# Kernel optimization log

Hardware: AMD Instinct MI355X
Metric: run time of the kernel (lower is better)

The kernel has to match this reference:

```python
import jax, jax.numpy as jnp
import numpy as np

LSP_ORDER = 32
RATE = 0.01
N_ITER = 4
MIN_D = RATE * np.pi / (LSP_ORDER + 1)  # _precompute


def setup_inputs() -> dict:
    key = jax.random.key(0)
    # LSP coefficients in radians, valid range (0, pi)
    w = jax.random.uniform(key, (256, 4096, LSP_ORDER + 1), dtype=jnp.float32,
                           minval=0.0, maxval=float(np.pi))
    return {"w": w}


def reference(w):
    min_d = jnp.asarray(MIN_D, w.dtype)
    pi = jnp.asarray(np.pi, w.dtype)
    K, w1 = w[..., :1], w[..., 1:]  # (..., 1), (..., M)

    def one_pass(w1):
        # Sequential left-to-right repair: each pair (m, m+1) is pushed apart
        # by half the deficit; the updated right element feeds the next step.
        wt = jnp.moveaxis(w1, -1, 0)  # (M, ...)

        def step(c, nxt):
            s = 0.5 * jnp.maximum(min_d - (nxt - c), 0.0)
            return nxt + s, c - s  # carry = updated w1[m+1], out = final w1[m]

        c_last, outs = jax.lax.scan(step, wt[0], wt[1:])
        w1n = jnp.concatenate([outs, c_last[None]], axis=0)  # (M, ...)
        return jnp.clip(jnp.moveaxis(w1n, 0, -1), min_d, pi - min_d)

    # Early-exit break in the original is a no-op once converged (step sizes
    # become 0 and clip is idempotent), so running all N_ITER is exact.
    for _ in range(N_ITER):
        w1 = one_pass(w1)

    return jnp.concatenate([K, w1], axis=-1)
```

## Files before the change

kernel.cpp:

```cpp
#include <hip/hip_runtime.h>
#include <math.h>


#define ROWS 128
#define THREADS 128
#define ROW 33
#define FPB (ROWS * ROW)
#define V4PB (FPB / 4)

typedef const __attribute__((address_space(1))) unsigned int* gas_p;
typedef __attribute__((address_space(3))) unsigned int* las_p;

__global__ __launch_bounds__(THREADS) void lsp_stability_kernel(
    const float* __restrict__ in, float* __restrict__ out)
{
    __shared__ alignas(16) float smem[FPB];
    const int tid = threadIdx.x;
    const long long base = (long long)blockIdx.x * FPB;

    const float* gin = in + base;
    float4* out4 = (float4*)(out + base);
    float4* s4 = (float4*)smem;

    gas_p g = (gas_p)gin;
    las_p s = (las_p)smem;
#pragma unroll
    for (int j = 0; j < 8; ++j)
        __builtin_amdgcn_global_load_lds(g + (size_t)(tid + j * THREADS) * 4,
                                         s + (size_t)(tid + j * THREADS) * 4,
                                         16, 0, 0);
    if (tid < (V4PB - 8 * THREADS))
        __builtin_amdgcn_global_load_lds(g + (size_t)(tid + 8 * THREADS) * 4,
                                         s + (size_t)(tid + 8 * THREADS) * 4,
                                         16, 0, 0);
    __syncthreads();

    const float MIND = (float)(0.01 * M_PI / 33.0);
    const float PI_F = (float)M_PI;
    const float HI = PI_F - MIND;

    float w[32];
    float* row = smem + tid * ROW;
#pragma unroll
    for (int k = 0; k < 32; ++k) w[k] = row[k + 1];

#pragma unroll
    for (int it = 0; it < 4; ++it) {
        float c = w[0];
#pragma unroll
        for (int k = 1; k < 32; ++k) {
            float nxt = w[k];
            float sft = 0.5f * fmaxf(MIND - (nxt - c), 0.0f);
            w[k - 1] = c - sft;
            c = nxt + sft;
        }
        w[31] = c;
#pragma unroll
        for (int k = 0; k < 32; ++k)
            w[k] = fminf(fmaxf(w[k], MIND), HI);
    }

#pragma unroll
    for (int k = 0; k < 32; ++k) row[k + 1] = w[k];
    __syncthreads();

#pragma unroll
    for (int j = 0; j < 8; ++j)
        out4[tid + j * THREADS] = s4[tid + j * THREADS];
    if (tid < (V4PB - 8 * THREADS))
        out4[tid + 8 * THREADS] = s4[tid + 8 * THREADS];
}

extern "C" void kernel_launch(void* const* d_in, const int* in_sizes, int n_in,
                              void* d_out, int out_size, void* d_ws, size_t ws_size,
                              hipStream_t stream) {
    const float* in = (const float*)d_in[0];
    float* out = (float*)d_out;
    const int blocks = in_sizes[0] / FPB;
    lsp_stability_kernel<<<blocks, THREADS, 0, stream>>>(in, out);
}
```

Baseline: 237.3 us.

## Make kernel persistent with double-buffered LDS prefetch of the next tile

Blocks shrink to a single 64-thread wave, and the grid is capped at 2048 persistent blocks that loop over tiles. While the current tile is being processed, the next tile is prefetched into a second LDS buffer with global_load_lds. Hand-written s_waitcnt vmcnt values order the prefetch against the outstanding stores, which lets the block-wide barriers go. This aims to hide global load latency behind the serial repair arithmetic. The trade-off is fewer resident waves per CU and waitcnt values that depend on exact instruction counts.

```diff
diff --git a/kernel.cpp b/kernel.cpp
--- a/kernel.cpp
+++ b/kernel.cpp
@@ -2,73 +2,93 @@
 #include <math.h>
 
 
-#define ROWS 128
-#define THREADS 128
+#define THREADS 64
 #define ROW 33
-#define FPB (ROWS * ROW)
-#define V4PB (FPB / 4)
+#define TROWS 64
+#define FPT (TROWS * ROW)
+#define V4PT (FPT / 4)
+#define GRID 2048
 
 typedef const __attribute__((address_space(1))) unsigned int* gas_p;
 typedef __attribute__((address_space(3))) unsigned int* las_p;
 
-__global__ __launch_bounds__(THREADS) void lsp_stability_kernel(
-    const float* __restrict__ in, float* __restrict__ out)
+__device__ __forceinline__ void stage_tile(const float* __restrict__ gin,
+                                           las_p s, int tid)
 {
-    __shared__ alignas(16) float smem[FPB];
-    const int tid = threadIdx.x;
-    const long long base = (long long)blockIdx.x * FPB;
-
-    const float* gin = in + base;
-    float4* out4 = (float4*)(out + base);
-    float4* s4 = (float4*)smem;
-
     gas_p g = (gas_p)gin;
-    las_p s = (las_p)smem;
 #pragma unroll
     for (int j = 0; j < 8; ++j)
         __builtin_amdgcn_global_load_lds(g + (size_t)(tid + j * THREADS) * 4,
                                          s + (size_t)(tid + j * THREADS) * 4,
                                          16, 0, 0);
-    if (tid < (V4PB - 8 * THREADS))
+    if (tid < (V4PT - 8 * THREADS))
         __builtin_amdgcn_global_load_lds(g + (size_t)(tid + 8 * THREADS) * 4,
                                          s + (size_t)(tid + 8 * THREADS) * 4,
                                          16, 0, 0);
-    __syncthreads();
+}
+
+__global__ __launch_bounds__(THREADS) void lsp_stability_kernel(
+    const float* __restrict__ in, float* __restrict__ out, int tiles)
+{
+    __shared__ alignas(16) float smem[2][FPT];
+    const int tid = threadIdx.x;
+    const int bid = blockIdx.x;
+    if (bid >= tiles) return;
+    const int grid = (int)gridDim.x;
+    const int nt = (tiles - bid + grid - 1) / grid;
 
     const float MIND = (float)(0.01 * M_PI / 33.0);
     const float PI_F = (float)M_PI;
     const float HI = PI_F - MIND;
 
-    float w[32];
-    float* row = smem + tid * ROW;
+    stage_tile(in + (size_t)bid * FPT, (las_p)&smem[0][0], tid);
+
+    for (int t = 0; t < nt; ++t) {
+        const size_t tile = (size_t)bid + (size_t)t * grid;
+        const int cur = t & 1;
+
+        if (t + 1 < nt)
+            stage_tile(in + (tile + grid) * FPT, (las_p)&smem[cur ^ 1][0], tid);
+
+        if (t > 0 && t + 1 < nt)
+            asm volatile("s_waitcnt vmcnt(18)" ::: "memory");
+        else if (t == 0 && t + 1 == nt)
+            asm volatile("s_waitcnt vmcnt(0)" ::: "memory");
+        else
+            asm volatile("s_waitcnt vmcnt(9)" ::: "memory");
+
+        float w[32];
+        float* row = &smem[cur][0] + tid * ROW;
 #pragma unroll
-    for (int k = 0; k < 32; ++k) w[k] = row[k + 1];
+        for (int k = 0; k < 32; ++k) w[k] = row[k + 1];
 
 #pragma unroll
-    for (int it = 0; it < 4; ++it) {
-        float c = w[0];
+        for (int it = 0; it < 4; ++it) {
+            float c = w[0];
 #pragma unroll
-        for (int k = 1; k < 32; ++k) {
-            float nxt = w[k];
-            float sft = 0.5f * fmaxf(MIND - (nxt - c), 0.0f);
-            w[k - 1] = c - sft;
-            c = nxt + sft;
+            for (int k = 1; k < 32; ++k) {
+                float nxt = w[k];
+                float sft = 0.5f * fmaxf(MIND - (nxt - c), 0.0f);
+                w[k - 1] = c - sft;
+                c = nxt + sft;
+            }
+            w[31] = c;
+#pragma unroll
+            for (int k = 0; k < 32; ++k)
+                w[k] = fminf(fmaxf(w[k], MIND), HI);
         }
-        w[31] = c;
-#pragma unroll
-        for (int k = 0; k < 32; ++k)
-            w[k] = fminf(fmaxf(w[k], MIND), HI);
-    }
 
 #pragma unroll
-    for (int k = 0; k < 32; ++k) row[k + 1] = w[k];
-    __syncthreads();
+        for (int k = 0; k < 32; ++k) row[k + 1] = w[k];
 
+        float4* out4 = (float4*)(out + tile * FPT);
+        const float4* s4 = (const float4*)&smem[cur][0];
 #pragma unroll
-    for (int j = 0; j < 8; ++j)
-        out4[tid + j * THREADS] = s4[tid + j * THREADS];
-    if (tid < (V4PB - 8 * THREADS))
-        out4[tid + 8 * THREADS] = s4[tid + 8 * THREADS];
+        for (int j = 0; j < 8; ++j)
+            out4[tid + j * THREADS] = s4[tid + j * THREADS];
+        if (tid < (V4PT - 8 * THREADS))
+            out4[tid + 8 * THREADS] = s4[tid + 8 * THREADS];
+    }
 }
 
 extern "C" void kernel_launch(void* const* d_in, const int* in_sizes, int n_in,
@@ -76,6 +96,7 @@
                               hipStream_t stream) {
     const float* in = (const float*)d_in[0];
     float* out = (float*)d_out;
-    const int blocks = in_sizes[0] / FPB;
-    lsp_stability_kernel<<<blocks, THREADS, 0, stream>>>(in, out);
+    const int tiles = in_sizes[0] / FPT;
+    const int blocks = tiles < GRID ? tiles : GRID;
+    lsp_stability_kernel<<<blocks, THREADS, 0, stream>>>(in, out, tiles);
 }
```

Result: no change. 238.5 us (+0.5%).
